# Kernel tuning notes

Measured on AMD Instinct MI355X. Metric: run time of the kernel, lower is better.

## Reference

```python
import jax, jax.numpy as jnp
import numpy as np

E = 8        # n_routed_experts
Z = 4        # zero_expert_num (identity experts)
K = 2        # moe_topk
SCALE = 2.5  # routed_scaling_factor
T, H, I = 8192, 1024, 512


def setup_inputs() -> dict:
    key = jax.random.key(0)
    k0, k1, k2, k3, k4 = jax.random.split(key, 5)
    return {
        "hidden_states": jax.random.normal(k0, (T, H), jnp.float32),
        "router_w": jax.random.normal(k1, (E + Z, H), jnp.float32) * 0.02,
        "correction_bias": jax.random.normal(k2, (E + Z,), jnp.float32) * 0.01,
        "w13": jax.random.normal(k3, (E, 2 * I, H), jnp.float32) * 0.02,
        "w2": jax.random.normal(k4, (E, H, I), jnp.float32) * 0.02,
    }


def reference(hidden_states, router_w, correction_bias, w13, w2):
    # ---- router (float32) ----
    logits = hidden_states.astype(jnp.float32) @ router_w.T          # [T, E+Z]
    scores = jax.nn.softmax(logits, axis=-1)
    # correction bias only affects expert *selection*, not the gate weights
    _, topk_idx = jax.lax.top_k(scores + correction_bias, K)          # [T, K]
    topk_w = jnp.take_along_axis(scores, topk_idx, axis=-1)          # renormalize=False

    # ---- zero experts (identity type): idx >= E contributes scale * x ----
    is_zero = topk_idx >= E                                           # [T, K]
    routed_w = jnp.where(is_zero, 0.0, topk_w)
    zero_scale = jnp.where(is_zero, topk_w, 0.0).sum(-1, keepdims=True)
    zero_result = zero_scale * hidden_states                          # [T, H]

    # ---- combine weights per routed expert: [T, E] ----
    tok = jnp.arange(hidden_states.shape[0])[:, None]
    safe_idx = jnp.clip(topk_idx, 0, E - 1)   # zero-expert slots carry weight 0
    combine = jnp.zeros((hidden_states.shape[0], E), scores.dtype)
    combine = combine.at[tok, safe_idx].add(routed_w)

    # ---- grouped expert GEMMs (SiLU gated MLP), combined densely ----
    h = jnp.einsum('th,eih->eti', hidden_states, w13)                 # [E, T, 2I]
    g, u = jnp.split(h, 2, axis=-1)
    act = jax.nn.silu(g) * u                                          # [E, T, I]
    eo = jnp.einsum('eti,ehi->eth', act, w2)                          # [E, T, H]
    routed = jnp.einsum('te,eth->th', combine, eo)                    # [T, H]

    return routed * SCALE + zero_result
```

## Files before the change

kernel.cpp:

```cpp
#include <hip/hip_runtime.h>
#include <hip/hip_bf16.h>
#include <math.h>

typedef __bf16 bf16_t;
typedef bf16_t bf16x4 __attribute__((ext_vector_type(4)));
typedef bf16_t bf16x8 __attribute__((ext_vector_type(8)));
typedef float f32x4 __attribute__((ext_vector_type(4)));

#define T_TOK 8192
#define HDIM  1024
#define IDIM  512
#define NEXP  8
#define NTOT  12
#define MAXROWS (2 * T_TOK + NEXP * 128)
#define MAX_MTILES (MAXROWS / 128)

__device__ __forceinline__ void gll16(const bf16_t* g, bf16_t* l) {
  __builtin_amdgcn_global_load_lds((__attribute__((address_space(1))) void*)g,
                                   (__attribute__((address_space(3))) void*)l,
                                   16, 0, 0);
}

__global__ void wcast_init_kernel(const float* __restrict__ w13, const float* __restrict__ w2,
                                  bf16_t* __restrict__ w13b, bf16_t* __restrict__ w2b,
                                  int* __restrict__ sel_tok, float* __restrict__ sel_w) {
  size_t gid = (size_t)blockIdx.x * blockDim.x + threadIdx.x;
  if (gid < MAXROWS) { sel_tok[gid] = 0; sel_w[gid] = 0.f; }
  const size_t n13 = (size_t)NEXP * 2 * IDIM * HDIM / 8;
  const size_t n2  = (size_t)NEXP * HDIM * IDIM / 8;
  const float* in; bf16_t* out; size_t i;
  if (gid < n13)            { in = w13; out = w13b; i = gid * 8; }
  else if (gid < n13 + n2)  { in = w2;  out = w2b;  i = (gid - n13) * 8; }
  else return;
  float4 a = *(const float4*)&in[i];
  float4 b = *(const float4*)&in[i + 4];
  bf16x8 o;
  o[0] = (bf16_t)a.x; o[1] = (bf16_t)a.y; o[2] = (bf16_t)a.z; o[3] = (bf16_t)a.w;
  o[4] = (bf16_t)b.x; o[5] = (bf16_t)b.y; o[6] = (bf16_t)b.z; o[7] = (bf16_t)b.w;
  *(bf16x8*)&out[i] = o;
}

__global__ void router_kernel(const float* __restrict__ x, const float* __restrict__ rw,
                              const float* __restrict__ bias,
                              int* __restrict__ tk_e, float* __restrict__ tk_w,
                              bf16_t* __restrict__ xb, float* __restrict__ out) {
  int t = blockIdx.x;
  int l = threadIdx.x;
  const float4* xr = (const float4*)(x + (size_t)t * HDIM);
  float4 xv[4];
#pragma unroll
  for (int i = 0; i < 4; i++) xv[i] = xr[l + 64 * i];
#pragma unroll
  for (int i = 0; i < 4; i++) {
    bf16x4 o;
    o[0] = (bf16_t)xv[i].x; o[1] = (bf16_t)xv[i].y;
    o[2] = (bf16_t)xv[i].z; o[3] = (bf16_t)xv[i].w;
    *(bf16x4*)&xb[(size_t)t * HDIM + (size_t)(l + 64 * i) * 4] = o;
  }
  float part[NTOT];
#pragma unroll
  for (int e = 0; e < NTOT; e++) {
    const float4* wr = (const float4*)(rw + (size_t)e * HDIM);
    float s = 0.f;
#pragma unroll
    for (int i = 0; i < 4; i++) {
      float4 w = wr[l + 64 * i];
      s += xv[i].x * w.x + xv[i].y * w.y + xv[i].z * w.z + xv[i].w * w.w;
    }
    part[e] = s;
  }
#pragma unroll
  for (int off = 32; off > 0; off >>= 1)
#pragma unroll
    for (int e = 0; e < NTOT; e++) part[e] += __shfl_down(part[e], off);

  float zs = 0.f;
  if (l == 0) {
    float mx = part[0];
#pragma unroll
    for (int e = 1; e < NTOT; e++) mx = fmaxf(mx, part[e]);
    float p[NTOT], den = 0.f;
#pragma unroll
    for (int e = 0; e < NTOT; e++) { p[e] = expf(part[e] - mx); den += p[e]; }
    float inv = 1.f / den;
#pragma unroll
    for (int e = 0; e < NTOT; e++) p[e] *= inv;
    float s0 = -1e30f, s1 = -1e30f; int i0 = 0, i1 = 0;
#pragma unroll
    for (int e = 0; e < NTOT; e++) {
      float v = p[e] + bias[e];
      if (v > s0) { s1 = s0; i1 = i0; s0 = v; i0 = e; }
      else if (v > s1) { s1 = v; i1 = e; }
    }
    int idx[2] = { i0, i1 };
#pragma unroll
    for (int k = 0; k < 2; k++) {
      int e = idx[k];
      float w = p[e];
      if (e >= NEXP) { zs += w; tk_e[2 * t + k] = -1; tk_w[2 * t + k] = 0.f; }
      else           { tk_e[2 * t + k] = e; tk_w[2 * t + k] = w; }
    }
  }
  zs = __shfl(zs, 0);
#pragma unroll
  for (int i = 0; i < 4; i++) {
    float4 o = make_float4(zs * xv[i].x, zs * xv[i].y, zs * xv[i].z, zs * xv[i].w);
    *(float4*)&out[(size_t)t * HDIM + (size_t)(l + 64 * i) * 4] = o;
  }
}

__global__ void countscan_kernel(const int* __restrict__ tk_e, int* __restrict__ cursor,
                                 int* __restrict__ total_rows, int* __restrict__ tile_e,
                                 int* __restrict__ tile_p0, int* __restrict__ n_mtiles) {
  __shared__ int lc[NEXP];
  int tid = threadIdx.x;
  if (tid < NEXP) lc[tid] = 0;
  __syncthreads();
  int cnt[NEXP];
#pragma unroll
  for (int j = 0; j < NEXP; j++) cnt[j] = 0;
  for (int i = tid; i < 2 * T_TOK; i += 256) {
    int e = tk_e[i];
#pragma unroll
    for (int j = 0; j < NEXP; j++) cnt[j] += (e == j) ? 1 : 0;
  }
#pragma unroll
  for (int off = 32; off > 0; off >>= 1)
#pragma unroll
    for (int j = 0; j < NEXP; j++) cnt[j] += __shfl_down(cnt[j], off);
  if ((tid & 63) == 0)
#pragma unroll
    for (int j = 0; j < NEXP; j++) atomicAdd(&lc[j], cnt[j]);
  __syncthreads();
  if (tid == 0) {
    int run = 0, nt = 0;
    for (int e = 0; e < NEXP; e++) {
      cursor[e] = run;
      int ntile = (lc[e] + 127) / 128;
      for (int i = 0; i < ntile; i++) {
        tile_e[nt] = e;
        tile_p0[nt] = run + i * 128;
        nt++;
      }
      run += ntile * 128;
    }
    *total_rows = run;
    *n_mtiles = nt;
  }
}

__global__ void assign_kernel(const int* __restrict__ tk_e, const float* __restrict__ tk_w,
                              int* __restrict__ cursor, int* __restrict__ sel_tok,
                              float* __restrict__ sel_w) {
  __shared__ int lc[NEXP];
  __shared__ int lbase[NEXP];
  int tid = threadIdx.x;
  if (tid < NEXP) lc[tid] = 0;
  __syncthreads();
  int t = blockIdx.x * blockDim.x + tid;
  int e0 = tk_e[2 * t], e1 = tk_e[2 * t + 1];
  int r0 = (e0 >= 0) ? atomicAdd(&lc[e0], 1) : -1;
  int r1 = (e1 >= 0) ? atomicAdd(&lc[e1], 1) : -1;
  __syncthreads();
  if (tid < NEXP) lbase[tid] = atomicAdd(&cursor[tid], lc[tid]);
  __syncthreads();
  if (e0 >= 0) { int p = lbase[e0] + r0; sel_tok[p] = t; sel_w[p] = 2.5f * tk_w[2 * t]; }
  if (e1 >= 0) { int p = lbase[e1] + r1; sel_tok[p] = t; sel_w[p] = 2.5f * tk_w[2 * t + 1]; }
}

__global__ __launch_bounds__(256, 2) void gemm1_kernel(
    const bf16_t* __restrict__ xb, const bf16_t* __restrict__ w13b,
    const int* __restrict__ sel_tok, const int* __restrict__ tile_e,
    const int* __restrict__ tile_p0, const int* __restrict__ n_mtiles,
    bf16_t* __restrict__ actb) {
  const int ti = blockIdx.x;
  if (ti >= *n_mtiles) return;
  const int e = tile_e[ti];
  const int p0 = tile_p0[ti];
  const int g0 = blockIdx.y * 128;

  __shared__ alignas(16) bf16_t As[128 * 64];
  __shared__ alignas(16) bf16_t Bs[256 * 64];
  const int tid = threadIdx.x;
  const int w = tid >> 6, l = tid & 63;
  const int wr = w >> 1, wc = w & 1;
  const int quad = l >> 4, c16 = l & 15;

  const int srow = tid >> 3;
  const int csrc = ((tid & 7) ^ (srow & 7)) * 8;
  const bf16_t* w13e = w13b + (size_t)e * (2 * IDIM) * HDIM;
  const bf16_t* Asrc[4];
  const bf16_t* Bsrc[8];
#pragma unroll
  for (int s = 0; s < 4; s++) {
    int tok = sel_tok[p0 + s * 32 + srow];
    Asrc[s] = xb + (size_t)tok * HDIM + csrc;
  }
#pragma unroll
  for (int s = 0; s < 8; s++) {
    int col = g0 + (s >> 1) * 32 + srow + ((s & 1) ? IDIM : 0);
    Bsrc[s] = w13e + (size_t)col * HDIM + csrc;
  }

  f32x4 acc[4][8];
#pragma unroll
  for (int i = 0; i < 4; i++)
#pragma unroll
    for (int j = 0; j < 8; j++) acc[i][j] = (f32x4){0.f, 0.f, 0.f, 0.f};

  for (int k0 = 0; k0 < HDIM; k0 += 64) {
#pragma unroll
    for (int s = 0; s < 4; s++) gll16(Asrc[s] + k0, &As[s * 2048 + w * 512]);
#pragma unroll
    for (int s = 0; s < 8; s++) gll16(Bsrc[s] + k0, &Bs[s * 2048 + w * 512]);
    __syncthreads();
#pragma unroll
    for (int kk = 0; kk < 2; kk++) {
      const int kch = ((kk * 4 + quad) ^ (c16 & 7)) * 8;
      bf16x8 af[4], bfv[8];
#pragma unroll
      for (int mt = 0; mt < 4; mt++)
        af[mt] = *(const bf16x8*)&As[(wr * 64 + mt * 16 + c16) * 64 + kch];
#pragma unroll
      for (int nt = 0; nt < 8; nt++)
        bfv[nt] = *(const bf16x8*)&Bs[(wc * 128 + nt * 16 + c16) * 64 + kch];
#pragma unroll
      for (int mt = 0; mt < 4; mt++)
#pragma unroll
        for (int nt = 0; nt < 8; nt++)
          acc[mt][nt] = __builtin_amdgcn_mfma_f32_16x16x32_bf16(af[mt], bfv[nt], acc[mt][nt], 0, 0, 0);
    }
    __syncthreads();
  }

#pragma unroll
  for (int mt = 0; mt < 4; mt++) {
    int rowb = p0 + wr * 64 + mt * 16 + quad * 4;
#pragma unroll
    for (int ntg = 0; ntg < 4; ntg++) {
      int nt = (ntg & 1) + (ntg >> 1) * 4;
      int col = g0 + (wc * 2 + (nt >> 2)) * 32 + (nt & 1) * 16 + c16;
#pragma unroll
      for (int r = 0; r < 4; r++) {
        float g = acc[mt][nt][r];
        float u = acc[mt][nt + 2][r];
        float s = g / (1.f + expf(-g));
        actb[(size_t)(rowb + r) * IDIM + col] = (bf16_t)(s * u);
      }
    }
  }
}

__global__ __launch_bounds__(256, 2) void gemm2_kernel(
    const bf16_t* __restrict__ actb, const bf16_t* __restrict__ w2b,
    const float* __restrict__ sel_w, const int* __restrict__ sel_tok,
    const int* __restrict__ tile_e, const int* __restrict__ tile_p0,
    const int* __restrict__ n_mtiles, float* __restrict__ out) {
  const int ti = blockIdx.x;
  if (ti >= *n_mtiles) return;
  const int e = tile_e[ti];
  const int p0 = tile_p0[ti];
  const int n0 = blockIdx.y * 256;

  __shared__ alignas(16) bf16_t As[128 * 64];
  __shared__ alignas(16) bf16_t Bs[256 * 64];
  const int tid = threadIdx.x;
  const int w = tid >> 6, l = tid & 63;
  const int wr = w >> 1, wc = w & 1;
  const int quad = l >> 4, c16 = l & 15;

  const int srow = tid >> 3;
  const int csrc = ((tid & 7) ^ (srow & 7)) * 8;
  const bf16_t* w2e = w2b + (size_t)e * HDIM * IDIM;
  const bf16_t* Asrc[4];
  const bf16_t* Bsrc[8];
#pragma unroll
  for (int s = 0; s < 4; s++)
    Asrc[s] = actb + (size_t)(p0 + s * 32 + srow) * IDIM + csrc;
#pragma unroll
  for (int s = 0; s < 8; s++)
    Bsrc[s] = w2e + (size_t)(n0 + s * 32 + srow) * IDIM + csrc;

  f32x4 acc[4][8];
#pragma unroll
  for (int i = 0; i < 4; i++)
#pragma unroll
    for (int j = 0; j < 8; j++) acc[i][j] = (f32x4){0.f, 0.f, 0.f, 0.f};

  for (int k0 = 0; k0 < IDIM; k0 += 64) {
#pragma unroll
    for (int s = 0; s < 4; s++) gll16(Asrc[s] + k0, &As[s * 2048 + w * 512]);
#pragma unroll
    for (int s = 0; s < 8; s++) gll16(Bsrc[s] + k0, &Bs[s * 2048 + w * 512]);
    __syncthreads();
#pragma unroll
    for (int kk = 0; kk < 2; kk++) {
      const int kch = ((kk * 4 + quad) ^ (c16 & 7)) * 8;
      bf16x8 af[4], bfv[8];
#pragma unroll
      for (int mt = 0; mt < 4; mt++)
        af[mt] = *(const bf16x8*)&As[(wr * 64 + mt * 16 + c16) * 64 + kch];
#pragma unroll
      for (int nt = 0; nt < 8; nt++)
        bfv[nt] = *(const bf16x8*)&Bs[(wc * 128 + nt * 16 + c16) * 64 + kch];
#pragma unroll
      for (int mt = 0; mt < 4; mt++)
#pragma unroll
        for (int nt = 0; nt < 8; nt++)
          acc[mt][nt] = __builtin_amdgcn_mfma_f32_16x16x32_bf16(af[mt], bfv[nt], acc[mt][nt], 0, 0, 0);
    }
    __syncthreads();
  }

#pragma unroll
  for (int mt = 0; mt < 4; mt++) {
    int rowb = p0 + wr * 64 + mt * 16 + quad * 4;
#pragma unroll
    for (int r = 0; r < 4; r++) {
      float cw = sel_w[rowb + r];
      if (cw == 0.f) continue;
      int tok = sel_tok[rowb + r];
      float* orow = out + (size_t)tok * HDIM;
#pragma unroll
      for (int nt = 0; nt < 8; nt++) {
        int col = n0 + wc * 128 + nt * 16 + c16;
        atomicAdd(&orow[col], cw * acc[mt][nt][r]);
      }
    }
  }
}

extern "C" void kernel_launch(void* const* d_in, const int* in_sizes, int n_in,
                              void* d_out, int out_size, void* d_ws, size_t ws_size,
                              hipStream_t stream) {
  const float* x    = (const float*)d_in[0];
  const float* rw   = (const float*)d_in[1];
  const float* bias = (const float*)d_in[2];
  const float* w13  = (const float*)d_in[3];
  const float* w2   = (const float*)d_in[4];
  float* out = (float*)d_out;

  char* ws = (char*)d_ws;
  bf16_t* w13b = (bf16_t*)ws;  ws += (size_t)NEXP * 2 * IDIM * HDIM * 2;
  bf16_t* w2b  = (bf16_t*)ws;  ws += (size_t)NEXP * HDIM * IDIM * 2;
  bf16_t* xb   = (bf16_t*)ws;  ws += (size_t)T_TOK * HDIM * 2;
  bf16_t* actb = (bf16_t*)ws;  ws += (size_t)MAXROWS * IDIM * 2;
  int*   tk_e    = (int*)ws;   ws += (size_t)T_TOK * 2 * 4;
  float* tk_w    = (float*)ws; ws += (size_t)T_TOK * 2 * 4;
  int*   sel_tok = (int*)ws;   ws += (size_t)MAXROWS * 4;
  float* sel_w   = (float*)ws; ws += (size_t)MAXROWS * 4;
  int*   cursor  = (int*)ws;   ws += NEXP * 4;
  int*   total_rows = (int*)ws; ws += 4;
  int*   tile_e  = (int*)ws;   ws += MAX_MTILES * 4;
  int*   tile_p0 = (int*)ws;   ws += MAX_MTILES * 4;
  int*   n_mtiles = (int*)ws;  ws += 4;

  {
    size_t n8 = (size_t)NEXP * 2 * IDIM * HDIM / 8 + (size_t)NEXP * HDIM * IDIM / 8;
    wcast_init_kernel<<<(n8 + 255) / 256, 256, 0, stream>>>(w13, w2, w13b, w2b,
                                                            sel_tok, sel_w);
  }
  router_kernel<<<T_TOK, 64, 0, stream>>>(x, rw, bias, tk_e, tk_w, xb, out);
  countscan_kernel<<<1, 256, 0, stream>>>(tk_e, cursor, total_rows,
                                          tile_e, tile_p0, n_mtiles);
  assign_kernel<<<T_TOK / 256, 256, 0, stream>>>(tk_e, tk_w, cursor, sel_tok, sel_w);

  gemm1_kernel<<<dim3(MAX_MTILES, (2 * IDIM) / 256), 256, 0, stream>>>(
      xb, w13b, sel_tok, tile_e, tile_p0, n_mtiles, actb);
  gemm2_kernel<<<dim3(MAX_MTILES, HDIM / 256), 256, 0, stream>>>(
      actb, w2b, sel_w, sel_tok, tile_e, tile_p0, n_mtiles, out);
}
```

Baseline: 255.7 us.

## Replace gemm2 atomic scatter with bf16 staging plus gather combine kernel

gemm2 now writes weighted expert outputs as bf16 rows to a staging buffer instead of issuing fp32 atomicAdds into the output. A new combine kernel gathers each token's two rows by recorded position and adds the zero-expert term, so the router no longer writes the output. The weight cast and the router are also merged into one launch, and both GEMMs remap block indices so consecutive blocks spread across XCDs. This adds an extra staging buffer of about 35MB written and read back, and rounds expert outputs to bf16 before summation.

```diff
diff --git a/kernel.cpp b/kernel.cpp
--- a/kernel.cpp
+++ b/kernel.cpp
@@ -14,6 +14,7 @@
 #define NTOT  12
 #define MAXROWS (2 * T_TOK + NEXP * 128)
 #define MAX_MTILES (MAXROWS / 128)
+#define WCAST_BLOCKS 6144
 
 __device__ __forceinline__ void gll16(const bf16_t* g, bf16_t* l) {
   __builtin_amdgcn_global_load_lds((__attribute__((address_space(1))) void*)g,
@@ -21,31 +22,32 @@
                                    16, 0, 0);
 }
 
-__global__ void wcast_init_kernel(const float* __restrict__ w13, const float* __restrict__ w2,
-                                  bf16_t* __restrict__ w13b, bf16_t* __restrict__ w2b,
-                                  int* __restrict__ sel_tok, float* __restrict__ sel_w) {
-  size_t gid = (size_t)blockIdx.x * blockDim.x + threadIdx.x;
-  if (gid < MAXROWS) { sel_tok[gid] = 0; sel_w[gid] = 0.f; }
-  const size_t n13 = (size_t)NEXP * 2 * IDIM * HDIM / 8;
-  const size_t n2  = (size_t)NEXP * HDIM * IDIM / 8;
-  const float* in; bf16_t* out; size_t i;
-  if (gid < n13)            { in = w13; out = w13b; i = gid * 8; }
-  else if (gid < n13 + n2)  { in = w2;  out = w2b;  i = (gid - n13) * 8; }
-  else return;
-  float4 a = *(const float4*)&in[i];
-  float4 b = *(const float4*)&in[i + 4];
-  bf16x8 o;
-  o[0] = (bf16_t)a.x; o[1] = (bf16_t)a.y; o[2] = (bf16_t)a.z; o[3] = (bf16_t)a.w;
-  o[4] = (bf16_t)b.x; o[5] = (bf16_t)b.y; o[6] = (bf16_t)b.z; o[7] = (bf16_t)b.w;
-  *(bf16x8*)&out[i] = o;
-}
-
-__global__ void router_kernel(const float* __restrict__ x, const float* __restrict__ rw,
-                              const float* __restrict__ bias,
-                              int* __restrict__ tk_e, float* __restrict__ tk_w,
-                              bf16_t* __restrict__ xb, float* __restrict__ out) {
-  int t = blockIdx.x;
-  int l = threadIdx.x;
+__global__ __launch_bounds__(256) void pre_kernel(
+    const float* __restrict__ w13, const float* __restrict__ w2,
+    const float* __restrict__ x, const float* __restrict__ rw,
+    const float* __restrict__ bias,
+    bf16_t* __restrict__ w13b, bf16_t* __restrict__ w2b, bf16_t* __restrict__ xb,
+    int* __restrict__ tk_e, float* __restrict__ tk_w, float* __restrict__ zscale,
+    int* __restrict__ sel_tok, float* __restrict__ sel_w) {
+  const int bid = blockIdx.x;
+  const int tid = threadIdx.x;
+  if (bid < WCAST_BLOCKS) {
+    size_t gid = (size_t)bid * 256 + tid;
+    if (gid < MAXROWS) { sel_tok[gid] = 0; sel_w[gid] = 0.f; }
+    const size_t n13 = (size_t)NEXP * 2 * IDIM * HDIM / 8;
+    const float* in; bf16_t* outp; size_t i;
+    if (gid < n13) { in = w13; outp = w13b; i = gid * 8; }
+    else           { in = w2;  outp = w2b;  i = (gid - n13) * 8; }
+    float4 a = *(const float4*)&in[i];
+    float4 b = *(const float4*)&in[i + 4];
+    bf16x8 o;
+    o[0] = (bf16_t)a.x; o[1] = (bf16_t)a.y; o[2] = (bf16_t)a.z; o[3] = (bf16_t)a.w;
+    o[4] = (bf16_t)b.x; o[5] = (bf16_t)b.y; o[6] = (bf16_t)b.z; o[7] = (bf16_t)b.w;
+    *(bf16x8*)&outp[i] = o;
+    return;
+  }
+  int t = (bid - WCAST_BLOCKS) * 4 + (tid >> 6);
+  int l = tid & 63;
   const float4* xr = (const float4*)(x + (size_t)t * HDIM);
   float4 xv[4];
 #pragma unroll
@@ -74,7 +76,6 @@
 #pragma unroll
     for (int e = 0; e < NTOT; e++) part[e] += __shfl_down(part[e], off);
 
-  float zs = 0.f;
   if (l == 0) {
     float mx = part[0];
 #pragma unroll
@@ -92,6 +93,7 @@
       if (v > s0) { s1 = s0; i1 = i0; s0 = v; i0 = e; }
       else if (v > s1) { s1 = v; i1 = e; }
     }
+    float zs = 0.f;
     int idx[2] = { i0, i1 };
 #pragma unroll
     for (int k = 0; k < 2; k++) {
@@ -100,12 +102,7 @@
       if (e >= NEXP) { zs += w; tk_e[2 * t + k] = -1; tk_w[2 * t + k] = 0.f; }
       else           { tk_e[2 * t + k] = e; tk_w[2 * t + k] = w; }
     }
-  }
-  zs = __shfl(zs, 0);
-#pragma unroll
-  for (int i = 0; i < 4; i++) {
-    float4 o = make_float4(zs * xv[i].x, zs * xv[i].y, zs * xv[i].z, zs * xv[i].w);
-    *(float4*)&out[(size_t)t * HDIM + (size_t)(l + 64 * i) * 4] = o;
+    zscale[t] = zs;
   }
 }
 
@@ -151,7 +148,7 @@
 
 __global__ void assign_kernel(const int* __restrict__ tk_e, const float* __restrict__ tk_w,
                               int* __restrict__ cursor, int* __restrict__ sel_tok,
-                              float* __restrict__ sel_w) {
+                              float* __restrict__ sel_w, int* __restrict__ pos) {
   __shared__ int lc[NEXP];
   __shared__ int lbase[NEXP];
   int tid = threadIdx.x;
@@ -164,8 +161,11 @@
   __syncthreads();
   if (tid < NEXP) lbase[tid] = atomicAdd(&cursor[tid], lc[tid]);
   __syncthreads();
-  if (e0 >= 0) { int p = lbase[e0] + r0; sel_tok[p] = t; sel_w[p] = 2.5f * tk_w[2 * t]; }
-  if (e1 >= 0) { int p = lbase[e1] + r1; sel_tok[p] = t; sel_w[p] = 2.5f * tk_w[2 * t + 1]; }
+  int p0 = -1, p1 = -1;
+  if (e0 >= 0) { p0 = lbase[e0] + r0; sel_tok[p0] = t; sel_w[p0] = 2.5f * tk_w[2 * t]; }
+  if (e1 >= 0) { p1 = lbase[e1] + r1; sel_tok[p1] = t; sel_w[p1] = 2.5f * tk_w[2 * t + 1]; }
+  pos[2 * t] = p0;
+  pos[2 * t + 1] = p1;
 }
 
 __global__ __launch_bounds__(256, 2) void gemm1_kernel(
@@ -173,11 +173,13 @@
     const int* __restrict__ sel_tok, const int* __restrict__ tile_e,
     const int* __restrict__ tile_p0, const int* __restrict__ n_mtiles,
     bf16_t* __restrict__ actb) {
-  const int ti = blockIdx.x;
+  const int b = blockIdx.x;
+  const int L = (b & 7) * 68 + (b >> 3);
+  const int ti = L % MAX_MTILES;
+  const int g0 = (L / MAX_MTILES) * 128;
   if (ti >= *n_mtiles) return;
   const int e = tile_e[ti];
   const int p0 = tile_p0[ti];
-  const int g0 = blockIdx.y * 128;
 
   __shared__ alignas(16) bf16_t As[128 * 64];
   __shared__ alignas(16) bf16_t Bs[256 * 64];
@@ -253,14 +255,16 @@
 
 __global__ __launch_bounds__(256, 2) void gemm2_kernel(
     const bf16_t* __restrict__ actb, const bf16_t* __restrict__ w2b,
-    const float* __restrict__ sel_w, const int* __restrict__ sel_tok,
-    const int* __restrict__ tile_e, const int* __restrict__ tile_p0,
-    const int* __restrict__ n_mtiles, float* __restrict__ out) {
-  const int ti = blockIdx.x;
+    const float* __restrict__ sel_w, const int* __restrict__ tile_e,
+    const int* __restrict__ tile_p0, const int* __restrict__ n_mtiles,
+    bf16_t* __restrict__ eob) {
+  const int b = blockIdx.x;
+  const int L = (b & 7) * 68 + (b >> 3);
+  const int ti = L % MAX_MTILES;
+  const int n0 = (L / MAX_MTILES) * 256;
   if (ti >= *n_mtiles) return;
   const int e = tile_e[ti];
   const int p0 = tile_p0[ti];
-  const int n0 = blockIdx.y * 256;
 
   __shared__ alignas(16) bf16_t As[128 * 64];
   __shared__ alignas(16) bf16_t Bs[256 * 64];
@@ -314,20 +318,44 @@
 
 #pragma unroll
   for (int mt = 0; mt < 4; mt++) {
-    int rowb = p0 + wr * 64 + mt * 16 + quad * 4;
-#pragma unroll
-    for (int r = 0; r < 4; r++) {
-      float cw = sel_w[rowb + r];
-      if (cw == 0.f) continue;
-      int tok = sel_tok[rowb + r];
-      float* orow = out + (size_t)tok * HDIM;
-#pragma unroll
-      for (int nt = 0; nt < 8; nt++) {
-        int col = n0 + wc * 128 + nt * 16 + c16;
-        atomicAdd(&orow[col], cw * acc[mt][nt][r]);
-      }
-    }
-  }
+    int rowb = wr * 64 + mt * 16 + quad * 4;
+    float cw[4];
+#pragma unroll
+    for (int r = 0; r < 4; r++) cw[r] = sel_w[p0 + rowb + r];
+#pragma unroll
+    for (int nt = 0; nt < 8; nt++) {
+      int col = n0 + wc * 128 + nt * 16 + c16;
+#pragma unroll
+      for (int r = 0; r < 4; r++)
+        eob[(size_t)(p0 + rowb + r) * HDIM + col] = (bf16_t)(cw[r] * acc[mt][nt][r]);
+    }
+  }
+}
+
+__global__ void combine_kernel(const float* __restrict__ x, const float* __restrict__ zscale,
+                               const int* __restrict__ pos, const bf16_t* __restrict__ eob,
+                               float* __restrict__ out) {
+  size_t gid = (size_t)blockIdx.x * blockDim.x + threadIdx.x;
+  size_t t = gid >> 7;
+  size_t j = (gid & 127) << 3;
+  float zs = zscale[t];
+  int p0 = pos[2 * t], p1 = pos[2 * t + 1];
+  float4 a = *(const float4*)&x[t * HDIM + j];
+  float4 b = *(const float4*)&x[t * HDIM + j + 4];
+  float o[8] = { zs * a.x, zs * a.y, zs * a.z, zs * a.w,
+                 zs * b.x, zs * b.y, zs * b.z, zs * b.w };
+  if (p0 >= 0) {
+    bf16x8 v = *(const bf16x8*)&eob[(size_t)p0 * HDIM + j];
+#pragma unroll
+    for (int k = 0; k < 8; k++) o[k] += (float)v[k];
+  }
+  if (p1 >= 0) {
+    bf16x8 v = *(const bf16x8*)&eob[(size_t)p1 * HDIM + j];
+#pragma unroll
+    for (int k = 0; k < 8; k++) o[k] += (float)v[k];
+  }
+  *(float4*)&out[t * HDIM + j] = make_float4(o[0], o[1], o[2], o[3]);
+  *(float4*)&out[t * HDIM + j + 4] = make_float4(o[4], o[5], o[6], o[7]);
 }
 
 extern "C" void kernel_launch(void* const* d_in, const int* in_sizes, int n_in,
@@ -345,8 +373,11 @@
   bf16_t* w2b  = (bf16_t*)ws;  ws += (size_t)NEXP * HDIM * IDIM * 2;
   bf16_t* xb   = (bf16_t*)ws;  ws += (size_t)T_TOK * HDIM * 2;
   bf16_t* actb = (bf16_t*)ws;  ws += (size_t)MAXROWS * IDIM * 2;
+  bf16_t* eob  = (bf16_t*)ws;  ws += (size_t)MAXROWS * HDIM * 2;
   int*   tk_e    = (int*)ws;   ws += (size_t)T_TOK * 2 * 4;
   float* tk_w    = (float*)ws; ws += (size_t)T_TOK * 2 * 4;
+  float* zscale  = (float*)ws; ws += (size_t)T_TOK * 4;
+  int*   pos     = (int*)ws;   ws += (size_t)T_TOK * 2 * 4;
   int*   sel_tok = (int*)ws;   ws += (size_t)MAXROWS * 4;
   float* sel_w   = (float*)ws; ws += (size_t)MAXROWS * 4;
   int*   cursor  = (int*)ws;   ws += NEXP * 4;
@@ -355,18 +386,17 @@
   int*   tile_p0 = (int*)ws;   ws += MAX_MTILES * 4;
   int*   n_mtiles = (int*)ws;  ws += 4;
 
-  {
-    size_t n8 = (size_t)NEXP * 2 * IDIM * HDIM / 8 + (size_t)NEXP * HDIM * IDIM / 8;
-    wcast_init_kernel<<<(n8 + 255) / 256, 256, 0, stream>>>(w13, w2, w13b, w2b,
-                                                            sel_tok, sel_w);
-  }
-  router_kernel<<<T_TOK, 64, 0, stream>>>(x, rw, bias, tk_e, tk_w, xb, out);
+  pre_kernel<<<WCAST_BLOCKS + T_TOK / 4, 256, 0, stream>>>(
+      w13, w2, x, rw, bias, w13b, w2b, xb, tk_e, tk_w, zscale, sel_tok, sel_w);
   countscan_kernel<<<1, 256, 0, stream>>>(tk_e, cursor, total_rows,
                                           tile_e, tile_p0, n_mtiles);
-  assign_kernel<<<T_TOK / 256, 256, 0, stream>>>(tk_e, tk_w, cursor, sel_tok, sel_w);
-
-  gemm1_kernel<<<dim3(MAX_MTILES, (2 * IDIM) / 256), 256, 0, stream>>>(
+  assign_kernel<<<T_TOK / 256, 256, 0, stream>>>(tk_e, tk_w, cursor, sel_tok, sel_w, pos);
+
+  gemm1_kernel<<<MAX_MTILES * ((2 * IDIM) / 256), 256, 0, stream>>>(
       xb, w13b, sel_tok, tile_e, tile_p0, n_mtiles, actb);
-  gemm2_kernel<<<dim3(MAX_MTILES, HDIM / 256), 256, 0, stream>>>(
-      actb, w2b, sel_w, sel_tok, tile_e, tile_p0, n_mtiles, out);
-}
+  gemm2_kernel<<<MAX_MTILES * (HDIM / 256), 256, 0, stream>>>(
+      actb, w2b, sel_w, tile_e, tile_p0, n_mtiles, eob);
+
+  combine_kernel<<<(size_t)T_TOK * HDIM / 8 / 256, 256, 0, stream>>>(
+      x, zscale, pos, eob, out);
+}
```

Result: slower. 270.5 us (+5.8%).
